# Optimization experiments

Hardware: AMD Instinct MI355X
Metric: run time of the kernel (lower is better)

## Reference

```python
import jax, jax.numpy as jnp
import numpy as np

D_MODEL = 2048
NUM_HEADS = 16
D_HEAD = D_MODEL // NUM_HEADS
ROPE_THETA = 10000.0
MAX_SEQ_LEN = 2048
NEG_INF = -1e30


def _rope_tables(seq_len):
    pos = jnp.arange(seq_len, dtype=jnp.float32)[:, None]          # [s,1]
    i = jnp.arange(0, D_HEAD, 2, dtype=jnp.float32)                 # [d/2]
    freqs = 1.0 / (ROPE_THETA ** (i / D_HEAD))
    angles = pos * freqs                                            # [s, d/2]
    return jnp.cos(angles), jnp.sin(angles)


def _apply_rope(x, cos, sin):
    # x: [b,h,s,d]; interleaved pairs: x1 = even dims, x2 = odd dims
    x1 = x[..., 0::2]
    x2 = x[..., 1::2]
    r1 = x1 * cos - x2 * sin
    r2 = x1 * sin + x2 * cos
    return jnp.stack([r1, r2], axis=-1).reshape(x.shape)


def setup_inputs() -> dict:
    key = jax.random.key(0)
    ks = jax.random.split(key, 5)
    b, s = 2, 2048
    scale = 1.0 / np.sqrt(D_MODEL)  # ~kaiming fan_in scale
    return {
        "x": jax.random.normal(ks[0], (b, s, D_MODEL), jnp.float32),
        "Wq": jax.random.normal(ks[1], (D_MODEL, D_MODEL), jnp.float32) * scale,
        "bq": jnp.zeros((D_MODEL,), jnp.float32),
        "Wk": jax.random.normal(ks[2], (D_MODEL, D_MODEL), jnp.float32) * scale,
        "bk": jnp.zeros((D_MODEL,), jnp.float32),
        "Wv": jax.random.normal(ks[3], (D_MODEL, D_MODEL), jnp.float32) * scale,
        "bv": jnp.zeros((D_MODEL,), jnp.float32),
        "Wo": jax.random.normal(ks[4], (D_MODEL, D_MODEL), jnp.float32) * scale,
        "bo": jnp.zeros((D_MODEL,), jnp.float32),
    }


def reference(x, Wq, bq, Wk, bk, Wv, bv, Wo, bo):
    b, s, _ = x.shape
    # QKV projections (torch Linear: y = x @ W.T + b)
    q = x @ Wq.T + bq
    k = x @ Wk.T + bk
    v = x @ Wv.T + bv
    # split heads: b s (h d) -> b h s d
    def split(t):
        return t.reshape(b, s, NUM_HEADS, D_HEAD).transpose(0, 2, 1, 3)
    q, k, v = split(q), split(k), split(v)
    # RoPE
    cos, sin = _rope_tables(s)
    q = _apply_rope(q, cos, sin)
    k = _apply_rope(k, cos, sin)
    # scaled dot-product attention with causal mask
    scores = jnp.einsum('bhqd,bhkd->bhqk', q, k) / jnp.sqrt(jnp.float32(D_HEAD))
    causal = jnp.tril(jnp.ones((s, s), dtype=bool))
    scores = jnp.where(causal[None, None], scores, NEG_INF)
    attn = jax.nn.softmax(scores, axis=-1)
    out = jnp.einsum('bhqk,bhkd->bhqd', attn, v)
    # merge heads and output projection
    out = out.transpose(0, 2, 1, 3).reshape(b, s, D_MODEL)
    return out @ Wo.T + bo
```

## Files before the change

### kernel.cpp

```cpp
#include <hip/hip_runtime.h>
#include <math.h>

#define D_MODEL 2048
#define NH 16
#define DH 128
#define SEQ 2048
#define NBH 32

typedef unsigned short u16;
typedef unsigned int u32;
typedef __attribute__((ext_vector_type(8))) short short8;
typedef __attribute__((ext_vector_type(4))) float floatx4;
typedef __attribute__((ext_vector_type(4))) unsigned short ushort4v;

__device__ __forceinline__ u16 f2bf(float f) {
  u32 u = __builtin_bit_cast(u32, f);
  return (u16)((u + 0x8000u) >> 16);
}
__device__ __forceinline__ float bf2f(u16 h) {
  return __builtin_bit_cast(float, (u32)h << 16);
}

__device__ __forceinline__ void async_load16(const u16* g, u16* l) {
  __builtin_amdgcn_global_load_lds(
      (const __attribute__((address_space(1))) void*)g,
      (__attribute__((address_space(3))) void*)l, 16, 0, 0);
}

template <int CTRL>
__device__ __forceinline__ float dpp_mov(float x) {
  return __builtin_bit_cast(
      float, __builtin_amdgcn_update_dpp(0, __builtin_bit_cast(int, x), CTRL,
                                         0xf, 0xf, false));
}
__device__ __forceinline__ float rmax16(float x) {
  x = fmaxf(x, dpp_mov<0x121>(x));
  x = fmaxf(x, dpp_mov<0x122>(x));
  x = fmaxf(x, dpp_mov<0x124>(x));
  x = fmaxf(x, dpp_mov<0x128>(x));
  return x;
}

__global__ void cvt_kernel(const float* __restrict__ src, u16* __restrict__ dst,
                           int n) {
  const int i = (blockIdx.x * 256 + threadIdx.x) * 8;
  if (i >= n) return;
  const floatx4 a = *(const floatx4*)(src + i);
  const floatx4 b = *(const floatx4*)(src + i + 4);
  short8 h;
  h[0] = (short)f2bf(a[0]); h[1] = (short)f2bf(a[1]);
  h[2] = (short)f2bf(a[2]); h[3] = (short)f2bf(a[3]);
  h[4] = (short)f2bf(b[0]); h[5] = (short)f2bf(b[1]);
  h[6] = (short)f2bf(b[2]); h[7] = (short)f2bf(b[3]);
  *(short8*)(dst + i) = h;
}

__global__ __launch_bounds__(256, 2) void gemm_async(
    const u16* __restrict__ A, const u16* __restrict__ W0,
    const u16* __restrict__ W1, const u16* __restrict__ W2,
    const float* __restrict__ b0, const float* __restrict__ b1,
    const float* __restrict__ b2, void* __restrict__ C0, void* __restrict__ C1,
    void* __restrict__ C2, const int qkv) {
  __shared__ u16 As[128 * 64];
  __shared__ u16 Bs[128 * 64];
  const int tid = threadIdx.x;
  const int wave = tid >> 6, lane = tid & 63;
  const int lr = lane & 15, lg = lane >> 4;
  const int m0 = blockIdx.y * 128;
  const int wm = (wave & 1) * 64, wn = (wave >> 1) * 64;

  int n0, mode;
  const u16* W;
  const float* bias;
  void* C;
  if (qkv) {
    const int which = blockIdx.x >> 4;
    n0 = (blockIdx.x & 15) * 128;
    W = which == 0 ? W0 : which == 1 ? W1 : W2;
    bias = which == 0 ? b0 : which == 1 ? b1 : b2;
    C = which == 0 ? C0 : which == 1 ? C1 : C2;
    mode = which;
  } else {
    n0 = blockIdx.x * 128;
    W = W0; bias = b0; C = C0; mode = 3;
  }

  floatx4 acc[4][4];
#pragma unroll
  for (int i = 0; i < 4; ++i)
#pragma unroll
    for (int j = 0; j < 4; ++j) {
      floatx4 z = {0.f, 0.f, 0.f, 0.f};
      acc[i][j] = z;
    }

  for (int kt = 0; kt < D_MODEL; kt += 64) {
#pragma unroll
    for (int p = 0; p < 4; ++p) {
      const int s = p * 256 + tid;
      const int row = s >> 3, c = s & 7;
      const int g = c ^ (row & 7);
      async_load16(A + (size_t)(m0 + row) * D_MODEL + kt + g * 8,
                   &As[(p * 256 + wave * 64) * 8]);
    }
#pragma unroll
    for (int p = 0; p < 4; ++p) {
      const int s = p * 256 + tid;
      const int row = s >> 3, c = s & 7;
      const int g = c ^ (row & 7);
      async_load16(W + (size_t)(n0 + row) * D_MODEL + kt + g * 8,
                   &Bs[(p * 256 + wave * 64) * 8]);
    }
    __syncthreads();

#pragma unroll
    for (int ks = 0; ks < 2; ++ks) {
      short8 af[4], bfr[4];
      const int ch = (ks * 4 + lg) ^ (lr & 7);
#pragma unroll
      for (int i = 0; i < 4; ++i)
        af[i] = *(const short8*)&As[(wm + 16 * i + lr) * 64 + ch * 8];
#pragma unroll
      for (int j = 0; j < 4; ++j)
        bfr[j] = *(const short8*)&Bs[(wn + 16 * j + lr) * 64 + ch * 8];
#pragma unroll
      for (int i = 0; i < 4; ++i)
#pragma unroll
        for (int j = 0; j < 4; ++j)
          acc[i][j] = __builtin_amdgcn_mfma_f32_16x16x32_bf16(af[i], bfr[j],
                                                              acc[i][j], 0, 0, 0);
    }
    __syncthreads();
  }

  float bj[4];
  int ncol[4];
#pragma unroll
  for (int j = 0; j < 4; ++j) {
    ncol[j] = n0 + wn + 16 * j + lr;
    bj[j] = bias[ncol[j]];
  }

  if (mode == 3) {
    float* Cf = (float*)C;
#pragma unroll
    for (int i = 0; i < 4; ++i)
#pragma unroll
      for (int r = 0; r < 4; ++r) {
        const int m = m0 + wm + 16 * i + lg * 4 + r;
#pragma unroll
        for (int j = 0; j < 4; ++j)
          Cf[(size_t)m * D_MODEL + ncol[j]] = acc[i][j][r] + bj[j];
      }
  } else if (mode == 2) {
    u16* Ch = (u16*)C;
#pragma unroll
    for (int i = 0; i < 4; ++i)
#pragma unroll
      for (int r = 0; r < 4; ++r) {
        const int m = m0 + wm + 16 * i + lg * 4 + r;
        const int b = m >> 11, s = m & (SEQ - 1);
#pragma unroll
        for (int j = 0; j < 4; ++j) {
          const int h = ncol[j] >> 7, d = ncol[j] & (DH - 1);
          Ch[((size_t)((b * NH + h) * DH + d)) * SEQ + s] =
              f2bf(acc[i][j][r] + bj[j]);
        }
      }
  } else {
    u16* Ch = (u16*)C;
#pragma unroll
    for (int i = 0; i < 4; ++i)
#pragma unroll
      for (int r = 0; r < 4; ++r) {
        const int m = m0 + wm + 16 * i + lg * 4 + r;
        const int b = m >> 11, s = m & (SEQ - 1);
#pragma unroll
        for (int j = 0; j < 4; ++j) {
          const int h = ncol[j] >> 7, d = ncol[j] & (DH - 1);
          Ch[((size_t)((b * NH + h) * SEQ + s)) * DH + d] =
              f2bf(acc[i][j][r] + bj[j]);
        }
      }
  }
}

__global__ void rope_kernel(u16* __restrict__ Q, u16* __restrict__ K) {
  const int idx = blockIdx.x * blockDim.x + threadIdx.x;
  const int p = idx & 63;
  const int s = (idx >> 6) & (SEQ - 1);
  const int bh = idx >> 17;
  if (bh >= NBH) return;
  const float freq = exp2f(-(float)p * (13.287712379549449f / 64.0f));
  const float ang = (float)s * freq;
  float sn, cs;
  sincosf(ang, &sn, &cs);
  const size_t base = ((size_t)bh * SEQ + s) * DH + 2 * p;
  {
    const u32 qq = *(const u32*)(Q + base);
    const float x1 = bf2f((u16)(qq & 0xffffu)), x2 = bf2f((u16)(qq >> 16));
    *(u32*)(Q + base) =
        (u32)f2bf(x1 * cs - x2 * sn) | ((u32)f2bf(x1 * sn + x2 * cs) << 16);
  }
  {
    const u32 kk = *(const u32*)(K + base);
    const float x1 = bf2f((u16)(kk & 0xffffu)), x2 = bf2f((u16)(kk >> 16));
    *(u32*)(K + base) =
        (u32)f2bf(x1 * cs - x2 * sn) | ((u32)f2bf(x1 * sn + x2 * cs) << 16);
  }
}

__global__ __launch_bounds__(256, 2) void attn_kernel(
    const u16* __restrict__ Q, const u16* __restrict__ K,
    const u16* __restrict__ Vt, u16* __restrict__ Oflat) {
  __shared__ u16 Ks[64 * 128];
  __shared__ u16 Vts[128 * 64];
  __shared__ u16 Ps[4 * 32 * 72];
  const int tid = threadIdx.x;
  const int wave = tid >> 6, lane = tid & 63;
  const int lr = lane & 15, lg = lane >> 4;
  const int L = blockIdx.y * 16 + blockIdx.x;
  const int bh = L & 31;
  const int t = L >> 5;
  const int qt = (t < 8) ? t : 23 - t;
  const size_t qk0 = (size_t)bh * SEQ * DH;
  const int q0 = qt * 128 + wave * 32;
  const float C = 0.12752602f;
  const float RTHR = 62.7f;

  short8 qf[2][4];
#pragma unroll
  for (int i = 0; i < 2; ++i)
#pragma unroll
    for (int kb = 0; kb < 4; ++kb)
      qf[i][kb] = *(const short8*)(Q + qk0 + (size_t)(q0 + 16 * i + lr) * DH +
                                   kb * 32 + lg * 8);

  floatx4 o[2][9];
#pragma unroll
  for (int i = 0; i < 2; ++i)
#pragma unroll
    for (int jd = 0; jd < 9; ++jd) {
      floatx4 z = {0.f, 0.f, 0.f, 0.f};
      o[i][jd] = z;
    }
  float mrun[2][4];
#pragma unroll
  for (int i = 0; i < 2; ++i)
#pragma unroll
    for (int r = 0; r < 4; ++r) mrun[i][r] = -1e38f;

  const short8 onesv = {16256, 16256, 16256, 16256,
                        16256, 16256, 16256, 16256};

  u16* myP = &Ps[wave * 32 * 72];
  const int nkt = 2 * qt + 2;
  for (int kt = 0; kt < nkt; ++kt) {
#pragma unroll
    for (int p = 0; p < 4; ++p) {
      const int s = p * 256 + tid;
      const int row = s >> 4, c = s & 15;
      const int g = c ^ (row & 15);
      async_load16(K + qk0 + (size_t)(kt * 64 + row) * DH + g * 8,
                   &Ks[(p * 256 + wave * 64) * 8]);
    }
#pragma unroll
    for (int p = 0; p < 4; ++p) {
      const int s = p * 256 + tid;
      const int row = s >> 3, c = s & 7;
      const int g = c ^ (row & 7);
      async_load16(Vt + (size_t)bh * DH * SEQ + (size_t)row * SEQ + kt * 64 + g * 8,
                   &Vts[(p * 256 + wave * 64) * 8]);
    }
    __syncthreads();

    floatx4 sacc[2][4];
#pragma unroll
    for (int i = 0; i < 2; ++i)
#pragma unroll
      for (int j = 0; j < 4; ++j) {
        floatx4 z = {0.f, 0.f, 0.f, 0.f};
        sacc[i][j] = z;
      }
#pragma unroll
    for (int kb = 0; kb < 4; ++kb) {
      short8 kf[4];
#pragma unroll
      for (int j = 0; j < 4; ++j)
        kf[j] = *(const short8*)&Ks[(16 * j + lr) * 128 + (((kb * 4 + lg) ^ lr)) * 8];
      __builtin_amdgcn_s_setprio(1);
#pragma unroll
      for (int i = 0; i < 2; ++i)
#pragma unroll
        for (int j = 0; j < 4; ++j)
          sacc[i][j] = __builtin_amdgcn_mfma_f32_16x16x32_bf16(qf[i][kb], kf[j],
                                                               sacc[i][j], 0, 0, 0);
      __builtin_amdgcn_s_setprio(0);
    }

    if (kt >= 2 * qt) {
#pragma unroll
      for (int i = 0; i < 2; ++i)
#pragma unroll
        for (int j = 0; j < 4; ++j)
#pragma unroll
          for (int r = 0; r < 4; ++r) {
            const int kpos = kt * 64 + 16 * j + lr;
            const int qpos = q0 + 16 * i + lg * 4 + r;
            if (kpos > qpos) sacc[i][j][r] = -1e30f;
          }
    }

    float mx[2][4];
    float g = -1e38f;
#pragma unroll
    for (int i = 0; i < 2; ++i)
#pragma unroll
      for (int r = 0; r < 4; ++r) {
        float m = fmaxf(fmaxf(sacc[i][0][r], sacc[i][1][r]),
                        fmaxf(sacc[i][2][r], sacc[i][3][r]));
        m = rmax16(m);
        mx[i][r] = m;
        g = fmaxf(g, m - mrun[i][r]);
      }
    if (!__all(g <= RTHR)) {
#pragma unroll
      for (int i = 0; i < 2; ++i)
#pragma unroll
        for (int r = 0; r < 4; ++r) {
          const float mn = fmaxf(mrun[i][r], mx[i][r]);
          const float alpha = exp2f((mrun[i][r] - mn) * C);
          mrun[i][r] = mn;
#pragma unroll
          for (int jd = 0; jd < 9; ++jd) o[i][jd][r] *= alpha;
        }
    }
    float negMC[2][4];
#pragma unroll
    for (int i = 0; i < 2; ++i)
#pragma unroll
      for (int r = 0; r < 4; ++r) negMC[i][r] = -mrun[i][r] * C;

#pragma unroll
    for (int i = 0; i < 2; ++i)
#pragma unroll
      for (int j = 0; j < 4; ++j)
#pragma unroll
        for (int r = 0; r < 4; ++r) {
          const float pv = exp2f(fmaf(sacc[i][j][r], C, negMC[i][r]));
          myP[(16 * i + lg * 4 + r) * 72 + 16 * j + lr] = f2bf(pv);
        }

    asm volatile("s_waitcnt lgkmcnt(0)" ::: "memory");

#pragma unroll
    for (int kb = 0; kb < 2; ++kb) {
      short8 pf[2];
#pragma unroll
      for (int i = 0; i < 2; ++i)
        pf[i] = *(const short8*)&myP[(16 * i + lr) * 72 + kb * 32 + lg * 8];
      __builtin_amdgcn_s_setprio(1);
#pragma unroll
      for (int jd = 0; jd < 8; ++jd) {
        const short8 vf = *(const short8*)&Vts[(16 * jd + lr) * 64 +
                                               (((kb * 4 + lg) ^ (lr & 7))) * 8];
#pragma unroll
        for (int i = 0; i < 2; ++i)
          o[i][jd] = __builtin_amdgcn_mfma_f32_16x16x32_bf16(pf[i], vf, o[i][jd],
                                                             0, 0, 0);
      }
#pragma unroll
      for (int i = 0; i < 2; ++i)
        o[i][8] = __builtin_amdgcn_mfma_f32_16x16x32_bf16(pf[i], onesv, o[i][8],
                                                          0, 0, 0);
      __builtin_amdgcn_s_setprio(0);
    }
    __syncthreads();
  }

  const int b = bh >> 4, h = bh & (NH - 1);
#pragma unroll
  for (int i = 0; i < 2; ++i)
#pragma unroll
    for (int r = 0; r < 4; ++r) {
      const int qpos = q0 + 16 * i + lg * 4 + r;
      const float inv = 1.0f / o[i][8][r];
      u16* dst = Oflat + ((size_t)(b * SEQ + qpos)) * D_MODEL + h * DH;
#pragma unroll
      for (int jd = 0; jd < 8; ++jd) dst[16 * jd + lr] = f2bf(o[i][jd][r] * inv);
    }
}

template <int ABF16>
__global__ __launch_bounds__(256, 2) void gemm_kernel(
    const void* __restrict__ Aptr, const float* __restrict__ W,
    const float* __restrict__ bias, void* __restrict__ Cptr, const int mode) {
  __shared__ u16 As[128 * 72];
  __shared__ u16 Bs[128 * 72];
  const int tid = threadIdx.x;
  const int wave = tid >> 6, lane = tid & 63;
  const int lr = lane & 15, lg = lane >> 4;
  const int m0 = blockIdx.y * 128, n0 = blockIdx.x * 128;
  const int wm = (wave & 1) * 64, wn = (wave >> 1) * 64;

  floatx4 acc[4][4];
#pragma unroll
  for (int i = 0; i < 4; ++i)
#pragma unroll
    for (int j = 0; j < 4; ++j) {
      floatx4 z = {0.f, 0.f, 0.f, 0.f};
      acc[i][j] = z;
    }

  for (int kt = 0; kt < D_MODEL; kt += 64) {
    if (ABF16) {
      const u16* A = (const u16*)Aptr;
      const int row0 = tid >> 3, c8 = (tid & 7) * 8;
#pragma unroll
      for (int p = 0; p < 4; ++p) {
        const int row = row0 + p * 32;
        *(short8*)&As[row * 72 + c8] =
            *(const short8*)(A + (size_t)(m0 + row) * D_MODEL + kt + c8);
      }
    } else {
      const float* A = (const float*)Aptr;
      const int row0 = tid >> 4, c4 = (tid & 15) * 4;
#pragma unroll
      for (int p = 0; p < 8; ++p) {
        const int row = row0 + p * 16;
        const floatx4 v =
            *(const floatx4*)(A + (size_t)(m0 + row) * D_MODEL + kt + c4);
        ushort4v h;
        h[0] = f2bf(v[0]); h[1] = f2bf(v[1]); h[2] = f2bf(v[2]); h[3] = f2bf(v[3]);
        *(ushort4v*)&As[row * 72 + c4] = h;
      }
    }
    {
      const int row0 = tid >> 4, c4 = (tid & 15) * 4;
#pragma unroll
      for (int p = 0; p < 8; ++p) {
        const int row = row0 + p * 16;
        const floatx4 v =
            *(const floatx4*)(W + (size_t)(n0 + row) * D_MODEL + kt + c4);
        ushort4v h;
        h[0] = f2bf(v[0]); h[1] = f2bf(v[1]); h[2] = f2bf(v[2]); h[3] = f2bf(v[3]);
        *(ushort4v*)&Bs[row * 72 + c4] = h;
      }
    }
    __syncthreads();
#pragma unroll
    for (int ks = 0; ks < 2; ++ks) {
      short8 af[4], bfr[4];
#pragma unroll
      for (int i = 0; i < 4; ++i)
        af[i] = *(const short8*)&As[(wm + 16 * i + lr) * 72 + ks * 32 + lg * 8];
#pragma unroll
      for (int j = 0; j < 4; ++j)
        bfr[j] = *(const short8*)&Bs[(wn + 16 * j + lr) * 72 + ks * 32 + lg * 8];
#pragma unroll
      for (int i = 0; i < 4; ++i)
#pragma unroll
        for (int j = 0; j < 4; ++j)
          acc[i][j] = __builtin_amdgcn_mfma_f32_16x16x32_bf16(af[i], bfr[j],
                                                              acc[i][j], 0, 0, 0);
    }
    __syncthreads();
  }

  float bj[4];
  int ncol[4];
#pragma unroll
  for (int j = 0; j < 4; ++j) {
    ncol[j] = n0 + wn + 16 * j + lr;
    bj[j] = bias[ncol[j]];
  }

  if (mode == 3) {
    float* C = (float*)Cptr;
#pragma unroll
    for (int i = 0; i < 4; ++i)
#pragma unroll
      for (int r = 0; r < 4; ++r) {
        const int m = m0 + wm + 16 * i + lg * 4 + r;
#pragma unroll
        for (int j = 0; j < 4; ++j)
          C[(size_t)m * D_MODEL + ncol[j]] = acc[i][j][r] + bj[j];
      }
  } else if (mode == 2) {
    u16* C = (u16*)Cptr;
#pragma unroll
    for (int i = 0; i < 4; ++i)
#pragma unroll
      for (int r = 0; r < 4; ++r) {
        const int m = m0 + wm + 16 * i + lg * 4 + r;
        const int b = m >> 11, s = m & (SEQ - 1);
#pragma unroll
        for (int j = 0; j < 4; ++j) {
          const int h = ncol[j] >> 7, d = ncol[j] & (DH - 1);
          C[((size_t)((b * NH + h) * DH + d)) * SEQ + s] = f2bf(acc[i][j][r] + bj[j]);
        }
      }
  } else {
    u16* C = (u16*)Cptr;
#pragma unroll
    for (int i = 0; i < 4; ++i)
#pragma unroll
      for (int r = 0; r < 4; ++r) {
        const int m = m0 + wm + 16 * i + lg * 4 + r;
        const int b = m >> 11, s = m & (SEQ - 1);
#pragma unroll
        for (int j = 0; j < 4; ++j) {
          const int h = ncol[j] >> 7, d = ncol[j] & (DH - 1);
          C[((size_t)((b * NH + h) * SEQ + s)) * DH + d] = f2bf(acc[i][j][r] + bj[j]);
        }
      }
  }
}

extern "C" void kernel_launch(void* const* d_in, const int* in_sizes, int n_in,
                              void* d_out, int out_size, void* d_ws,
                              size_t ws_size, hipStream_t stream) {
  const float* x = (const float*)d_in[0];
  const float* Wq = (const float*)d_in[1];
  const float* bq = (const float*)d_in[2];
  const float* Wk = (const float*)d_in[3];
  const float* bk = (const float*)d_in[4];
  const float* Wv = (const float*)d_in[5];
  const float* bv = (const float*)d_in[6];
  const float* Wo = (const float*)d_in[7];
  const float* bo = (const float*)d_in[8];
  float* out = (float*)d_out;

  const size_t E = (size_t)NBH * SEQ * DH;
  const size_t WE = (size_t)D_MODEL * D_MODEL;
  const size_t need = (4 * E + 3 * WE) * sizeof(u16);

  const dim3 gb(256);

  if (ws_size >= need) {
    u16* xb = (u16*)d_ws;
    u16* wqb = xb + E;
    u16* wkb = wqb + WE;
    u16* wvb = wkb + WE;
    u16* q = wvb + WE;
    u16* k = q + E;
    u16* vt = k + E;
    u16* aflat = xb;
    u16* wob = q;

    cvt_kernel<<<dim3((int)(E / 2048)), gb, 0, stream>>>(x, xb, (int)E);
    cvt_kernel<<<dim3((int)(WE / 2048)), gb, 0, stream>>>(Wq, wqb, (int)WE);
    cvt_kernel<<<dim3((int)(WE / 2048)), gb, 0, stream>>>(Wk, wkb, (int)WE);
    cvt_kernel<<<dim3((int)(WE / 2048)), gb, 0, stream>>>(Wv, wvb, (int)WE);

    gemm_async<<<dim3(48, 32), gb, 0, stream>>>(xb, wqb, wkb, wvb, bq, bk, bv,
                                                q, k, vt, 1);
    rope_kernel<<<dim3((NBH * SEQ * (DH / 2)) / 256), gb, 0, stream>>>(q, k);
    attn_kernel<<<dim3(SEQ / 128, NBH), gb, 0, stream>>>(q, k, vt, aflat);
    cvt_kernel<<<dim3((int)(WE / 2048)), gb, 0, stream>>>(Wo, wob, (int)WE);
    gemm_async<<<dim3(16, 32), gb, 0, stream>>>(aflat, wob, nullptr, nullptr,
                                                bo, nullptr, nullptr, out,
                                                nullptr, nullptr, 0);
  } else {
    u16* q = (u16*)d_ws;
    u16* k = q + E;
    u16* vt = k + E;
    u16* aflat = vt + E;
    const dim3 gg(D_MODEL / 128, (2 * SEQ) / 128);
    gemm_kernel<0><<<gg, gb, 0, stream>>>(x, Wq, bq, q, 0);
    gemm_kernel<0><<<gg, gb, 0, stream>>>(x, Wk, bk, k, 1);
    gemm_kernel<0><<<gg, gb, 0, stream>>>(x, Wv, bv, vt, 2);
    rope_kernel<<<dim3((NBH * SEQ * (DH / 2)) / 256), dim3(256), 0, stream>>>(q, k);
    attn_kernel<<<dim3(SEQ / 128, NBH), gb, 0, stream>>>(q, k, vt, aflat);
    gemm_kernel<1><<<gg, gb, 0, stream>>>(aflat, Wo, bo, out, 3);
  }
}
```

Before: 395.9 us.

## Double-buffer K tiles, transpose score MFMA, and fuse input conversions

The attention kernel now double-buffers K tiles in shared memory, prefetching the next tile while the current one is computed. It also swaps the MFMA operands so each lane holds scores along the key dimension for a single query row. That lets the row max use two cross-lane shuffles instead of DPP reductions, lets P be written to LDS as packed 8-byte stores, and keeps only one running max per row. Separately, the four fp32-to-bf16 conversion launches are merged into one kernel to cut launch overhead. The costs are more LDS per block and extra shuffles when the accumulator is rescaled.

```diff
diff --git a/kernel.cpp b/kernel.cpp
--- a/kernel.cpp
+++ b/kernel.cpp
@@ -11,6 +11,7 @@
 typedef unsigned int u32;
 typedef __attribute__((ext_vector_type(8))) short short8;
 typedef __attribute__((ext_vector_type(4))) float floatx4;
+typedef __attribute__((ext_vector_type(2))) unsigned int uint2v;
 typedef __attribute__((ext_vector_type(4))) unsigned short ushort4v;
 
 __device__ __forceinline__ u16 f2bf(float f) {
@@ -27,24 +28,40 @@
       (__attribute__((address_space(3))) void*)l, 16, 0, 0);
 }
 
-template <int CTRL>
-__device__ __forceinline__ float dpp_mov(float x) {
-  return __builtin_bit_cast(
-      float, __builtin_amdgcn_update_dpp(0, __builtin_bit_cast(int, x), CTRL,
-                                         0xf, 0xf, false));
-}
-__device__ __forceinline__ float rmax16(float x) {
-  x = fmaxf(x, dpp_mov<0x121>(x));
-  x = fmaxf(x, dpp_mov<0x122>(x));
-  x = fmaxf(x, dpp_mov<0x124>(x));
-  x = fmaxf(x, dpp_mov<0x128>(x));
-  return x;
-}
-
 __global__ void cvt_kernel(const float* __restrict__ src, u16* __restrict__ dst,
                            int n) {
   const int i = (blockIdx.x * 256 + threadIdx.x) * 8;
   if (i >= n) return;
+  const floatx4 a = *(const floatx4*)(src + i);
+  const floatx4 b = *(const floatx4*)(src + i + 4);
+  short8 h;
+  h[0] = (short)f2bf(a[0]); h[1] = (short)f2bf(a[1]);
+  h[2] = (short)f2bf(a[2]); h[3] = (short)f2bf(a[3]);
+  h[4] = (short)f2bf(b[0]); h[5] = (short)f2bf(b[1]);
+  h[6] = (short)f2bf(b[2]); h[7] = (short)f2bf(b[3]);
+  *(short8*)(dst + i) = h;
+}
+
+__global__ void cvt4_kernel(const float* __restrict__ x,
+                            const float* __restrict__ wq,
+                            const float* __restrict__ wk,
+                            const float* __restrict__ wv, u16* __restrict__ xb,
+                            u16* __restrict__ wqb, u16* __restrict__ wkb,
+                            u16* __restrict__ wvb) {
+  const int blk = blockIdx.x;
+  const float* src;
+  u16* dst;
+  int base;
+  if (blk < 4096) {
+    src = x; dst = xb; base = blk;
+  } else if (blk < 6144) {
+    src = wq; dst = wqb; base = blk - 4096;
+  } else if (blk < 8192) {
+    src = wk; dst = wkb; base = blk - 6144;
+  } else {
+    src = wv; dst = wvb; base = blk - 8192;
+  }
+  const int i = (base * 256 + threadIdx.x) * 8;
   const floatx4 a = *(const floatx4*)(src + i);
   const floatx4 b = *(const floatx4*)(src + i + 4);
   short8 h;
@@ -213,7 +230,7 @@
 __global__ __launch_bounds__(256, 2) void attn_kernel(
     const u16* __restrict__ Q, const u16* __restrict__ K,
     const u16* __restrict__ Vt, u16* __restrict__ Oflat) {
-  __shared__ u16 Ks[64 * 128];
+  __shared__ u16 Ks[2][64 * 128];
   __shared__ u16 Vts[128 * 64];
   __shared__ u16 Ps[4 * 32 * 72];
   const int tid = threadIdx.x;
@@ -244,26 +261,27 @@
       floatx4 z = {0.f, 0.f, 0.f, 0.f};
       o[i][jd] = z;
     }
-  float mrun[2][4];
-#pragma unroll
-  for (int i = 0; i < 2; ++i)
-#pragma unroll
-    for (int r = 0; r < 4; ++r) mrun[i][r] = -1e38f;
+  float mrun[2] = {-1e38f, -1e38f};
 
   const short8 onesv = {16256, 16256, 16256, 16256,
                         16256, 16256, 16256, 16256};
 
   u16* myP = &Ps[wave * 32 * 72];
   const int nkt = 2 * qt + 2;
+
+#pragma unroll
+  for (int p = 0; p < 4; ++p) {
+    const int s = p * 256 + tid;
+    const int row = s >> 4, c = s & 15;
+    const int g = c ^ (row & 15);
+    async_load16(K + qk0 + (size_t)row * DH + g * 8,
+                 &Ks[0][(p * 256 + wave * 64) * 8]);
+  }
+  __syncthreads();
+
   for (int kt = 0; kt < nkt; ++kt) {
-#pragma unroll
-    for (int p = 0; p < 4; ++p) {
-      const int s = p * 256 + tid;
-      const int row = s >> 4, c = s & 15;
-      const int g = c ^ (row & 15);
-      async_load16(K + qk0 + (size_t)(kt * 64 + row) * DH + g * 8,
-                   &Ks[(p * 256 + wave * 64) * 8]);
-    }
+    const int cur = kt & 1, nb = cur ^ 1;
+    const int kn = (kt + 1 < nkt) ? kt + 1 : kt;
 #pragma unroll
     for (int p = 0; p < 4; ++p) {
       const int s = p * 256 + tid;
@@ -272,86 +290,107 @@
       async_load16(Vt + (size_t)bh * DH * SEQ + (size_t)row * SEQ + kt * 64 + g * 8,
                    &Vts[(p * 256 + wave * 64) * 8]);
     }
-    __syncthreads();
-
-    floatx4 sacc[2][4];
-#pragma unroll
-    for (int i = 0; i < 2; ++i)
-#pragma unroll
-      for (int j = 0; j < 4; ++j) {
+#pragma unroll
+    for (int p = 0; p < 4; ++p) {
+      const int s = p * 256 + tid;
+      const int row = s >> 4, c = s & 15;
+      const int g = c ^ (row & 15);
+      async_load16(K + qk0 + (size_t)(kn * 64 + row) * DH + g * 8,
+                   &Ks[nb][(p * 256 + wave * 64) * 8]);
+    }
+
+    floatx4 st[4][2];
+#pragma unroll
+    for (int j = 0; j < 4; ++j)
+#pragma unroll
+      for (int i = 0; i < 2; ++i) {
         floatx4 z = {0.f, 0.f, 0.f, 0.f};
-        sacc[i][j] = z;
+        st[j][i] = z;
       }
 #pragma unroll
     for (int kb = 0; kb < 4; ++kb) {
       short8 kf[4];
 #pragma unroll
       for (int j = 0; j < 4; ++j)
-        kf[j] = *(const short8*)&Ks[(16 * j + lr) * 128 + (((kb * 4 + lg) ^ lr)) * 8];
+        kf[j] = *(const short8*)&Ks[cur][(16 * j + lr) * 128 +
+                                         (((kb * 4 + lg) ^ lr)) * 8];
       __builtin_amdgcn_s_setprio(1);
 #pragma unroll
+      for (int j = 0; j < 4; ++j)
+#pragma unroll
+        for (int i = 0; i < 2; ++i)
+          st[j][i] = __builtin_amdgcn_mfma_f32_16x16x32_bf16(kf[j], qf[i][kb],
+                                                             st[j][i], 0, 0, 0);
+      __builtin_amdgcn_s_setprio(0);
+    }
+
+    if (kt >= 2 * qt) {
+#pragma unroll
+      for (int j = 0; j < 4; ++j)
+#pragma unroll
+        for (int i = 0; i < 2; ++i)
+#pragma unroll
+          for (int r = 0; r < 4; ++r) {
+            const int kpos = kt * 64 + 16 * j + 4 * lg + r;
+            const int qpos = q0 + 16 * i + lr;
+            if (kpos > qpos) st[j][i][r] = -1e30f;
+          }
+    }
+
+    float mx[2];
+#pragma unroll
+    for (int i = 0; i < 2; ++i) {
+      float m0v = fmaxf(fmaxf(st[0][i][0], st[0][i][1]),
+                        fmaxf(st[0][i][2], st[0][i][3]));
+      float m1v = fmaxf(fmaxf(st[1][i][0], st[1][i][1]),
+                        fmaxf(st[1][i][2], st[1][i][3]));
+      float m2v = fmaxf(fmaxf(st[2][i][0], st[2][i][1]),
+                        fmaxf(st[2][i][2], st[2][i][3]));
+      float m3v = fmaxf(fmaxf(st[3][i][0], st[3][i][1]),
+                        fmaxf(st[3][i][2], st[3][i][3]));
+      float m = fmaxf(fmaxf(m0v, m1v), fmaxf(m2v, m3v));
+      m = fmaxf(m, __shfl_xor(m, 16));
+      m = fmaxf(m, __shfl_xor(m, 32));
+      mx[i] = m;
+    }
+    const float grow = fmaxf(mx[0] - mrun[0], mx[1] - mrun[1]);
+    if (!__all(grow <= RTHR)) {
+      float aS[2];
+#pragma unroll
+      for (int i = 0; i < 2; ++i) {
+        const float mn = fmaxf(mrun[i], mx[i]);
+        aS[i] = exp2f((mrun[i] - mn) * C);
+        mrun[i] = mn;
+      }
+#pragma unroll
       for (int i = 0; i < 2; ++i)
 #pragma unroll
-        for (int j = 0; j < 4; ++j)
-          sacc[i][j] = __builtin_amdgcn_mfma_f32_16x16x32_bf16(qf[i][kb], kf[j],
-                                                               sacc[i][j], 0, 0, 0);
-      __builtin_amdgcn_s_setprio(0);
-    }
-
-    if (kt >= 2 * qt) {
-#pragma unroll
-      for (int i = 0; i < 2; ++i)
-#pragma unroll
-        for (int j = 0; j < 4; ++j)
-#pragma unroll
-          for (int r = 0; r < 4; ++r) {
-            const int kpos = kt * 64 + 16 * j + lr;
-            const int qpos = q0 + 16 * i + lg * 4 + r;
-            if (kpos > qpos) sacc[i][j][r] = -1e30f;
-          }
-    }
-
-    float mx[2][4];
-    float g = -1e38f;
+        for (int r = 0; r < 4; ++r) {
+          const float aO = __shfl(aS[i], 4 * lg + r);
+#pragma unroll
+          for (int jd = 0; jd < 9; ++jd) o[i][jd][r] *= aO;
+        }
+    }
+    float negMC[2];
+#pragma unroll
+    for (int i = 0; i < 2; ++i) negMC[i] = -mrun[i] * C;
+
 #pragma unroll
     for (int i = 0; i < 2; ++i)
 #pragma unroll
-      for (int r = 0; r < 4; ++r) {
-        float m = fmaxf(fmaxf(sacc[i][0][r], sacc[i][1][r]),
-                        fmaxf(sacc[i][2][r], sacc[i][3][r]));
-        m = rmax16(m);
-        mx[i][r] = m;
-        g = fmaxf(g, m - mrun[i][r]);
-      }
-    if (!__all(g <= RTHR)) {
-#pragma unroll
-      for (int i = 0; i < 2; ++i)
-#pragma unroll
-        for (int r = 0; r < 4; ++r) {
-          const float mn = fmaxf(mrun[i][r], mx[i][r]);
-          const float alpha = exp2f((mrun[i][r] - mn) * C);
-          mrun[i][r] = mn;
-#pragma unroll
-          for (int jd = 0; jd < 9; ++jd) o[i][jd][r] *= alpha;
-        }
-    }
-    float negMC[2][4];
-#pragma unroll
-    for (int i = 0; i < 2; ++i)
-#pragma unroll
-      for (int r = 0; r < 4; ++r) negMC[i][r] = -mrun[i][r] * C;
-
-#pragma unroll
-    for (int i = 0; i < 2; ++i)
-#pragma unroll
-      for (int j = 0; j < 4; ++j)
-#pragma unroll
-        for (int r = 0; r < 4; ++r) {
-          const float pv = exp2f(fmaf(sacc[i][j][r], C, negMC[i][r]));
-          myP[(16 * i + lg * 4 + r) * 72 + 16 * j + lr] = f2bf(pv);
-        }
+      for (int j = 0; j < 4; ++j) {
+        const float p0 = exp2f(fmaf(st[j][i][0], C, negMC[i]));
+        const float p1 = exp2f(fmaf(st[j][i][1], C, negMC[i]));
+        const float p2 = exp2f(fmaf(st[j][i][2], C, negMC[i]));
+        const float p3 = exp2f(fmaf(st[j][i][3], C, negMC[i]));
+        uint2v w;
+        w[0] = (u32)f2bf(p0) | ((u32)f2bf(p1) << 16);
+        w[1] = (u32)f2bf(p2) | ((u32)f2bf(p3) << 16);
+        *(uint2v*)&myP[(16 * i + lr) * 72 + 16 * j + 4 * lg] = w;
+      }
 
     asm volatile("s_waitcnt lgkmcnt(0)" ::: "memory");
+    __syncthreads();
 
 #pragma unroll
     for (int kb = 0; kb < 2; ++kb) {
@@ -548,10 +587,8 @@
     u16* aflat = xb;
     u16* wob = q;
 
-    cvt_kernel<<<dim3((int)(E / 2048)), gb, 0, stream>>>(x, xb, (int)E);
-    cvt_kernel<<<dim3((int)(WE / 2048)), gb, 0, stream>>>(Wq, wqb, (int)WE);
-    cvt_kernel<<<dim3((int)(WE / 2048)), gb, 0, stream>>>(Wk, wkb, (int)WE);
-    cvt_kernel<<<dim3((int)(WE / 2048)), gb, 0, stream>>>(Wv, wvb, (int)WE);
+    cvt4_kernel<<<dim3(10240), gb, 0, stream>>>(x, Wq, Wk, Wv, xb, wqb, wkb,
+                                                wvb);
 
     gemm_async<<<dim3(48, 32), gb, 0, stream>>>(xb, wqb, wkb, wvb, bq, bk, bv,
                                                 q, k, vt, 1);
```

Result: faster. 382.4 us (-3.4%).
